# Optimization experiments

Measured on AMD Instinct MI355X. Metric: run time of the kernel, lower is better.

The kernel has to match this reference:

```python
import jax, jax.numpy as jnp
import numpy as np
from jax import lax

H = 1024       # hidden_size
I = 1024       # intermediate_size (per expert)
E = 16         # num_experts
TOP_K = 4      # num_active_experts


def setup_inputs() -> dict:
    key = jax.random.key(0)
    ks = jax.random.split(key, 9)
    std_gate = 0.02 / (E ** 0.5)
    return {
        "hidden_states": jax.random.normal(ks[0], (1, 2048, H), jnp.float32),
        "gate_w": jax.random.normal(ks[1], (E, H), jnp.float32) * std_gate,
        "expert_bias": jnp.zeros((E,), jnp.float32),
        "w1": jax.random.normal(ks[2], (E, I, H), jnp.float32) * 0.02,
        "w2": jax.random.normal(ks[3], (E, H, I), jnp.float32) * 0.02,
        "w3": jax.random.normal(ks[4], (E, I, H), jnp.float32) * 0.02,
        "sw1": jax.random.normal(ks[5], (I, H), jnp.float32) * 0.02,
        "sw2": jax.random.normal(ks[6], (H, I), jnp.float32) * 0.02,
        "sw3": jax.random.normal(ks[7], (I, H), jnp.float32) * 0.02,
    }


def _swiglu(x, wg, wd, wu):
    # Swish(x W1^T) * (x W3^T) then W2^T
    return (jax.nn.silu(x @ wg.T) * (x @ wu.T)) @ wd.T


def reference(hidden_states, gate_w, expert_bias, w1, w2, w3, sw1, sw2, sw3):
    B, S, Hd = hidden_states.shape
    x = hidden_states.reshape(-1, Hd)              # [T, H]
    T = x.shape[0]

    # ---- Router ----
    router_logits = x @ gate_w.T                   # [T, E]
    biased = router_logits + expert_bias           # loss-free balancing bias
    _, sel = lax.top_k(biased, TOP_K)              # [T, K] indices from biased logits
    raw = jnp.take_along_axis(router_logits, sel, axis=-1)  # weights from UNbiased logits
    rw = jax.nn.softmax(raw.astype(jnp.float32), axis=-1).astype(x.dtype)  # [T, K]

    # Dense combine weights g[t, e] = routing weight if e selected else 0
    g = jnp.zeros((T, E), x.dtype).at[jnp.arange(T)[:, None], sel].add(rw)

    # ---- Routed experts (mathematically equal to grouped dispatch) ----
    routed = jnp.zeros_like(x)
    for e in range(E):  # fixed small expert loop
        routed = routed + g[:, e:e + 1] * _swiglu(x, w1[e], w2[e], w3[e])

    # ---- Shared expert ----
    shared = _swiglu(x, sw1, sw2, sw3)

    out = (shared + routed).reshape(B, S, Hd)      # dropout p=0 -> identity
    return out
```

## Files before the change

### kernel.cpp

```cpp
#include <hip/hip_runtime.h>
#include <cstddef>
#include <cstdint>

#define T_TOK 2048
#define HD 1024
#define ID 1024
#define NE 16
#define TOPK 4
#define BM 128
#define BN 128
#define BK 32
#define MT_MAX 96
#define SLOT_CAP (MT_MAX * BM)

typedef float f32x4 __attribute__((ext_vector_type(4)));
typedef __bf16 bf16x8 __attribute__((ext_vector_type(8)));
typedef __bf16 bf16x4 __attribute__((ext_vector_type(4)));

#define WS_TILE_E 256
#define WS_LOGITS 4096
#define WS_SLOT_TOK (WS_LOGITS + T_TOK * NE * 4)
#define WS_SLOT_W (WS_SLOT_TOK + SLOT_CAP * 4)
#define WS_H1 (WS_SLOT_W + SLOT_CAP * 4)
#define WS_XB (WS_H1 + (size_t)SLOT_CAP * ID * 2)

__device__ __forceinline__ f32x4 mfma16(bf16x8 a, bf16x8 b, f32x4 c) {
  return __builtin_amdgcn_mfma_f32_16x16x32_bf16(a, b, c, 0, 0, 0);
}

__device__ __forceinline__ bf16x8 pack8(f32x4 a, f32x4 b) {
  bf16x8 o;
  o[0] = (__bf16)a[0]; o[1] = (__bf16)a[1]; o[2] = (__bf16)a[2]; o[3] = (__bf16)a[3];
  o[4] = (__bf16)b[0]; o[5] = (__bf16)b[1]; o[6] = (__bf16)b[2]; o[7] = (__bf16)b[3];
  return o;
}

__device__ __forceinline__ bf16x4 pack4(f32x4 a) {
  bf16x4 o;
  o[0] = (__bf16)a[0]; o[1] = (__bf16)a[1]; o[2] = (__bf16)a[2]; o[3] = (__bf16)a[3];
  return o;
}

__device__ __forceinline__ void gload16(const __bf16* g, __bf16* l) {
  __builtin_amdgcn_global_load_lds(
      (const __attribute__((address_space(1))) uint32_t*)g,
      (__attribute__((address_space(3))) uint32_t*)l, 16, 0, 0);
}
__device__ __forceinline__ void gload16f(const float* g, float* l) {
  __builtin_amdgcn_global_load_lds(
      (const __attribute__((address_space(1))) uint32_t*)g,
      (__attribute__((address_space(3))) uint32_t*)l, 16, 0, 0);
}

#define LOGITS_BLOCKS (T_TOK / 4)
#define XCHUNKS 256

__global__ __launch_bounds__(256) void fused_pre(
    const float* __restrict__ x, const float* __restrict__ gw,
    __bf16* __restrict__ xb, float* __restrict__ logits) {
  int tid = threadIdx.x;
  if ((int)blockIdx.x < LOGITS_BLOCKS) {
    int wv = tid >> 6;
    int lane = tid & 63;
    int tok = blockIdx.x * 4 + wv;
    int e = lane >> 2;
    int q = lane & 3;
    const float4* xr = (const float4*)(x + (size_t)tok * HD) + q * 64;
    const float4* wr = (const float4*)(gw + (size_t)e * HD) + q * 64;
    float s0 = 0.f, s1 = 0.f;
#pragma unroll 8
    for (int i = 0; i < 64; i += 2) {
      float4 a0 = xr[i], w0 = wr[i];
      float4 a1 = xr[i + 1], w1v = wr[i + 1];
      s0 += a0.x * w0.x + a0.y * w0.y + a0.z * w0.z + a0.w * w0.w;
      s1 += a1.x * w1v.x + a1.y * w1v.y + a1.z * w1v.z + a1.w * w1v.w;
    }
    float s = s0 + s1;
    s += __shfl_xor(s, 1);
    s += __shfl_xor(s, 2);
    if (q == 0) logits[(size_t)tok * NE + e] = s;
    return;
  }
  size_t f = (size_t)(blockIdx.x - LOGITS_BLOCKS) * 2048;
  const f32x4* p = (const f32x4*)x + f + tid;
  __bf16* q = xb + 4 * (f + tid);
  f32x4 v0 = p[0], v1 = p[256], v2 = p[512], v3 = p[768];
  f32x4 v4 = p[1024], v5 = p[1280], v6 = p[1536], v7 = p[1792];
  *(bf16x4*)(q + 0 * 1024) = pack4(v0);
  *(bf16x4*)(q + 1 * 1024) = pack4(v1);
  *(bf16x4*)(q + 2 * 1024) = pack4(v2);
  *(bf16x4*)(q + 3 * 1024) = pack4(v3);
  *(bf16x4*)(q + 4 * 1024) = pack4(v4);
  *(bf16x4*)(q + 5 * 1024) = pack4(v5);
  *(bf16x4*)(q + 6 * 1024) = pack4(v6);
  *(bf16x4*)(q + 7 * 1024) = pack4(v7);
}

__global__ __launch_bounds__(256) void router_finish(
    const float* __restrict__ logits, const float* __restrict__ bias,
    int* __restrict__ tile_e, int* __restrict__ slot_tok,
    float* __restrict__ slot_w) {
  __shared__ int hist[NE];
  __shared__ int soff[NE + 1];
  __shared__ int fillp[NE];
  __shared__ unsigned lsel[T_TOK];
  __shared__ float4 lw4[T_TOK];

  int tid = threadIdx.x;
  if (tid < NE) { hist[tid] = 0; fillp[tid] = 0; }
  __syncthreads();

  float bb[NE];
#pragma unroll
  for (int e = 0; e < NE; ++e) bb[e] = bias[e];

  for (int j = 0; j < T_TOK / 256; ++j) {
    int t = tid + 256 * j;
    float lg[NE];
    const float4* lp = (const float4*)(logits + (size_t)t * NE);
#pragma unroll
    for (int q = 0; q < 4; ++q) {
      float4 v = lp[q];
      lg[4 * q] = v.x; lg[4 * q + 1] = v.y; lg[4 * q + 2] = v.z; lg[4 * q + 3] = v.w;
    }
    float b[NE];
#pragma unroll
    for (int e = 0; e < NE; ++e) b[e] = lg[e] + bb[e];

    int selk[TOPK];
    float raw[TOPK];
    unsigned used = 0;
#pragma unroll
    for (int k = 0; k < TOPK; ++k) {
      float best = -3.4e38f;
      int bi = 0;
#pragma unroll
      for (int e = 0; e < NE; ++e) {
        if (!((used >> e) & 1) && b[e] > best) { best = b[e]; bi = e; }
      }
      used |= (1u << bi);
      selk[k] = bi;
      raw[k] = lg[bi];
    }
    float m = raw[0];
#pragma unroll
    for (int k = 1; k < TOPK; ++k) m = fmaxf(m, raw[k]);
    float s = 0.f;
    float w[TOPK];
#pragma unroll
    for (int k = 0; k < TOPK; ++k) { w[k] = __expf(raw[k] - m); s += w[k]; }
    float inv = 1.f / s;
    lsel[t] = (unsigned)selk[0] | ((unsigned)selk[1] << 8) |
              ((unsigned)selk[2] << 16) | ((unsigned)selk[3] << 24);
    lw4[t] = make_float4(w[0] * inv, w[1] * inv, w[2] * inv, w[3] * inv);
#pragma unroll
    for (int k = 0; k < TOPK; ++k) atomicAdd(&hist[selk[k]], 1);
  }
  __syncthreads();

  if (tid == 0) {
    int o = 0;
    for (int e = 0; e < NE; ++e) { soff[e] = o; o += (hist[e] + BM - 1) & ~(BM - 1); }
    soff[NE] = o;
  }
  __syncthreads();
  int shared_base = soff[NE];
  int total = shared_base + T_TOK;
  for (int tt = tid; tt < MT_MAX; tt += 256) {
    int base = tt * BM;
    int ee = -1;
    if (base < shared_base) {
      ee = 0;
#pragma unroll
      for (int q = 1; q < NE; ++q) if (base >= soff[q]) ee = q;
    } else if (base < total) {
      ee = NE;
    }
    tile_e[tt] = ee;
  }

  for (int j = 0; j < T_TOK / 256; ++j) {
    int t = tid + 256 * j;
    unsigned ps = lsel[t];
    float4 wv = lw4[t];
    int e0 = ps & 255, e1 = (ps >> 8) & 255, e2 = (ps >> 16) & 255, e3 = ps >> 24;
    int p0 = atomicAdd(&fillp[e0], 1);
    slot_tok[soff[e0] + p0] = t; slot_w[soff[e0] + p0] = wv.x;
    int p1 = atomicAdd(&fillp[e1], 1);
    slot_tok[soff[e1] + p1] = t; slot_w[soff[e1] + p1] = wv.y;
    int p2 = atomicAdd(&fillp[e2], 1);
    slot_tok[soff[e2] + p2] = t; slot_w[soff[e2] + p2] = wv.z;
    int p3 = atomicAdd(&fillp[e3], 1);
    slot_tok[soff[e3] + p3] = t; slot_w[soff[e3] + p3] = wv.w;
  }

  for (int s = tid; s < shared_base; s += 256) {
    int e = 0;
#pragma unroll
    for (int q = 1; q < NE; ++q) if (s >= soff[q]) e = q;
    if (s >= soff[e] + hist[e]) { slot_tok[s] = -1; slot_w[s] = 0.f; }
  }
  for (int s = shared_base + tid; s < total; s += 256) {
    slot_tok[s] = s - shared_base;
    slot_w[s] = 1.0f;
  }
}


__global__ __launch_bounds__(256, 2) void pass1_bf16(
    const __bf16* __restrict__ xb, const int* __restrict__ slot_tok,
    const int* __restrict__ tile_e, const float* __restrict__ w1,
    const float* __restrict__ w3, const float* __restrict__ sw1,
    const float* __restrict__ sw3, __bf16* __restrict__ h1) {
  int mt = blockIdx.y;
  int e = tile_e[mt];
  if (e < 0) return;
  int n0 = blockIdx.x * BN;
  int m0 = mt * BM;

  const float* wg = (e == NE) ? sw1 : w1 + (size_t)e * ID * HD;
  const float* wu = (e == NE) ? sw3 : w3 + (size_t)e * ID * HD;

  __shared__ __align__(16) __bf16 As[2][BM * BK];
  __shared__ __align__(16) float BgF[2][BN * BK];
  __shared__ __align__(16) float BuF[2][BN * BK];

  int tid = threadIdx.x;
  int r0 = tid >> 2, r1 = r0 + 64;
  int c8 = ((tid & 3) ^ ((r0 >> 1) & 3)) * 8;
  int tok0 = slot_tok[m0 + r0]; if (tok0 < 0) tok0 = 0;
  int tok1 = slot_tok[m0 + r1]; if (tok1 < 0) tok1 = 0;
  const __bf16* gA0 = xb + (size_t)tok0 * HD + c8;
  const __bf16* gA1 = xb + (size_t)tok1 * HD + c8;

  const float* srcG[4];
  const float* srcU[4];
  int ldst[4];
#pragma unroll
  for (int j = 0; j < 4; ++j) {
    int id = tid + j * 256;
    int r = id >> 3, s = id & 7;
    int go = (s ^ (r & 7)) << 2;
    srcG[j] = wg + (size_t)(n0 + r) * HD + go;
    srcU[j] = wu + (size_t)(n0 + r) * HD + go;
    ldst[j] = id * 4;
  }

  int wave = tid >> 6, lane = tid & 63;
  int wm = (wave >> 1) * 64, wn = (wave & 1) * 64;
  int l16 = lane & 15, kch = lane >> 4;
  int kk8 = (kch ^ ((l16 >> 1) & 3)) * 8;
  int sw = l16 & 7;
  int cB0 = ((2 * kch) ^ sw) * 4;
  int cB1 = ((2 * kch + 1) ^ sw) * 4;

  f32x4 accg[4][4] = {};
  f32x4 accu[4][4] = {};

  auto stage = [&](int B, int k0) {
    gload16(gA0 + k0, &As[B][(size_t)tid * 8]);
    gload16(gA1 + k0, &As[B][(size_t)(tid + 256) * 8]);
#pragma unroll
    for (int j = 0; j < 4; ++j) {
      gload16f(srcG[j] + k0, &BgF[B][ldst[j]]);
      gload16f(srcU[j] + k0, &BuF[B][ldst[j]]);
    }
  };
  auto body = [&](int B) {
    bf16x8 af[4], gf[4], uf[4];
#pragma unroll
    for (int i = 0; i < 4; ++i)
      af[i] = *(const bf16x8*)(&As[B][(wm + i * 16 + l16) * BK + kk8]);
#pragma unroll
    for (int i = 0; i < 4; ++i) {
      int rb = (wn + i * 16 + l16) * BK;
      f32x4 ga = *(const f32x4*)(&BgF[B][rb + cB0]);
      f32x4 gb = *(const f32x4*)(&BgF[B][rb + cB1]);
      gf[i] = pack8(ga, gb);
      f32x4 ua = *(const f32x4*)(&BuF[B][rb + cB0]);
      f32x4 ub = *(const f32x4*)(&BuF[B][rb + cB1]);
      uf[i] = pack8(ua, ub);
    }
    asm volatile("s_waitcnt lgkmcnt(0)" ::: "memory");
    __builtin_amdgcn_s_barrier();
    __builtin_amdgcn_sched_barrier(0);
#pragma unroll
    for (int mi = 0; mi < 4; ++mi)
#pragma unroll
      for (int ni = 0; ni < 4; ++ni) {
        accg[mi][ni] = mfma16(af[mi], gf[ni], accg[mi][ni]);
        accu[mi][ni] = mfma16(af[mi], uf[ni], accu[mi][ni]);
      }
  };

  stage(0, 0);
#pragma unroll 1
  for (int k = 0; k < HD / BK - 1; ++k) {
    int cur = k & 1;
    stage(cur ^ 1, (k + 1) * BK);
    asm volatile("s_waitcnt vmcnt(10)" ::: "memory");
    __builtin_amdgcn_s_barrier();
    __builtin_amdgcn_sched_barrier(0);
    body(cur);
  }
  asm volatile("s_waitcnt vmcnt(0)" ::: "memory");
  __builtin_amdgcn_s_barrier();
  __builtin_amdgcn_sched_barrier(0);
  body((HD / BK - 1) & 1);

#pragma unroll
  for (int mi = 0; mi < 4; ++mi) {
#pragma unroll
    for (int ni = 0; ni < 4; ++ni) {
#pragma unroll
      for (int j = 0; j < 4; ++j) {
        int row = m0 + wm + mi * 16 + kch * 4 + j;
        int col = n0 + wn + ni * 16 + l16;
        float g = accg[mi][ni][j];
        float u = accu[mi][ni][j];
        float hv = (g / (1.f + __expf(-g))) * u;
        h1[(size_t)row * ID + col] = (__bf16)hv;
      }
    }
  }
}

__global__ __launch_bounds__(256, 3) void pass2_bf16(
    const __bf16* __restrict__ h1, const int* __restrict__ slot_tok,
    const float* __restrict__ slot_w, const int* __restrict__ tile_e,
    const float* __restrict__ w2, const float* __restrict__ sw2,
    float* __restrict__ out) {
  int mt = blockIdx.y;
  int e = tile_e[mt];
  if (e < 0) return;
  int n0 = blockIdx.x * BN;
  int m0 = mt * BM;

  const float* wd = (e == NE) ? sw2 : w2 + (size_t)e * HD * ID;

  __shared__ __align__(16) __bf16 As[2][BM * BK];
  __shared__ __align__(16) float BF[2][BN * BK];

  int tid = threadIdx.x;
  int r0 = tid >> 2, r1 = r0 + 64;
  int c8 = ((tid & 3) ^ ((r0 >> 1) & 3)) * 8;
  const __bf16* gA0 = h1 + (size_t)(m0 + r0) * ID + c8;
  const __bf16* gA1 = h1 + (size_t)(m0 + r1) * ID + c8;

  const float* srcB[4];
  int ldst[4];
#pragma unroll
  for (int j = 0; j < 4; ++j) {
    int id = tid + j * 256;
    int r = id >> 3, s = id & 7;
    int go = (s ^ (r & 7)) << 2;
    srcB[j] = wd + (size_t)(n0 + r) * ID + go;
    ldst[j] = id * 4;
  }

  int wave = tid >> 6, lane = tid & 63;
  int wm = (wave >> 1) * 64, wn = (wave & 1) * 64;
  int l16 = lane & 15, kch = lane >> 4;
  int kk8 = (kch ^ ((l16 >> 1) & 3)) * 8;
  int sw = l16 & 7;
  int cB0 = ((2 * kch) ^ sw) * 4;
  int cB1 = ((2 * kch + 1) ^ sw) * 4;

  f32x4 acc[4][4] = {};

  auto stage = [&](int B, int k0) {
    gload16(gA0 + k0, &As[B][(size_t)tid * 8]);
    gload16(gA1 + k0, &As[B][(size_t)(tid + 256) * 8]);
#pragma unroll
    for (int j = 0; j < 4; ++j) gload16f(srcB[j] + k0, &BF[B][ldst[j]]);
  };
  auto body = [&](int B) {
    bf16x8 af[4], bf[4];
#pragma unroll
    for (int i = 0; i < 4; ++i)
      af[i] = *(const bf16x8*)(&As[B][(wm + i * 16 + l16) * BK + kk8]);
#pragma unroll
    for (int i = 0; i < 4; ++i) {
      int rb = (wn + i * 16 + l16) * BK;
      f32x4 ba = *(const f32x4*)(&BF[B][rb + cB0]);
      f32x4 bb = *(const f32x4*)(&BF[B][rb + cB1]);
      bf[i] = pack8(ba, bb);
    }
    asm volatile("s_waitcnt lgkmcnt(0)" ::: "memory");
    __builtin_amdgcn_s_barrier();
    __builtin_amdgcn_sched_barrier(0);
#pragma unroll
    for (int mi = 0; mi < 4; ++mi)
#pragma unroll
      for (int ni = 0; ni < 4; ++ni)
        acc[mi][ni] = mfma16(af[mi], bf[ni], acc[mi][ni]);
  };

  stage(0, 0);
#pragma unroll 1
  for (int k = 0; k < ID / BK - 1; ++k) {
    int cur = k & 1;
    stage(cur ^ 1, (k + 1) * BK);
    asm volatile("s_waitcnt vmcnt(6)" ::: "memory");
    __builtin_amdgcn_s_barrier();
    __builtin_amdgcn_sched_barrier(0);
    body(cur);
  }
  asm volatile("s_waitcnt vmcnt(0)" ::: "memory");
  __builtin_amdgcn_s_barrier();
  __builtin_amdgcn_sched_barrier(0);
  body((ID / BK - 1) & 1);

#pragma unroll
  for (int mi = 0; mi < 4; ++mi) {
#pragma unroll
    for (int j = 0; j < 4; ++j) {
      int row = m0 + wm + mi * 16 + kch * 4 + j;
      int token = slot_tok[row];
      if (token < 0) continue;
      float wgt = slot_w[row];
#pragma unroll
      for (int ni = 0; ni < 4; ++ni) {
        int col = n0 + wn + ni * 16 + l16;
        atomicAdd(out + (size_t)token * HD + col, wgt * acc[mi][ni][j]);
      }
    }
  }
}

extern "C" void kernel_launch(void* const* d_in, const int* in_sizes, int n_in,
                              void* d_out, int out_size, void* d_ws, size_t ws_size,
                              hipStream_t stream) {
  const float* x = (const float*)d_in[0];
  const float* gate_w = (const float*)d_in[1];
  const float* ebias = (const float*)d_in[2];
  const float* w1 = (const float*)d_in[3];
  const float* w2 = (const float*)d_in[4];
  const float* w3 = (const float*)d_in[5];
  const float* sw1 = (const float*)d_in[6];
  const float* sw2 = (const float*)d_in[7];
  const float* sw3 = (const float*)d_in[8];
  float* out = (float*)d_out;

  char* ws = (char*)d_ws;
  int* tile_e = (int*)(ws + WS_TILE_E);
  float* logits = (float*)(ws + WS_LOGITS);
  int* slot_tok = (int*)(ws + WS_SLOT_TOK);
  float* slot_w = (float*)(ws + WS_SLOT_W);
  __bf16* h1 = (__bf16*)(ws + WS_H1);
  __bf16* xb = (__bf16*)(ws + WS_XB);

  hipMemsetAsync(d_out, 0, (size_t)T_TOK * HD * sizeof(float), stream);

  fused_pre<<<LOGITS_BLOCKS + XCHUNKS, 256, 0, stream>>>(x, gate_w, xb, logits);
  router_finish<<<1, 256, 0, stream>>>(logits, ebias, tile_e, slot_tok, slot_w);

  pass1_bf16<<<dim3(ID / BN, MT_MAX), 256, 0, stream>>>(
      xb, slot_tok, tile_e, w1, w3, sw1, sw3, h1);
  pass2_bf16<<<dim3(HD / BN, MT_MAX), 256, 0, stream>>>(
      h1, slot_tok, slot_w, tile_e, w2, sw2, out);
}
```

Baseline: 223.8 us.

## Use 256-row, 512-thread tiles in pass1 to halve weight reloads

Expert segments are now padded to 256 rows, and pass1 runs 512-thread blocks that each cover 256 token slots by 128 columns, with a new tile-to-expert map for the larger tiles. Each block loads its fp32 gate and up weight tiles once for twice as many rows, halving weight traffic and bf16 conversion per token. Pass2 keeps 128-row tiles through the old map, which still lines up because every segment is a multiple of 128. The cost is more padding rows per expert, more LDS per block and more accumulator registers per wave, which may lower occupancy.

Result: slower. 245.6 us (+9.7%).

```diff
diff --git a/kernel.cpp b/kernel.cpp
--- a/kernel.cpp
+++ b/kernel.cpp
@@ -8,16 +8,19 @@
 #define NE 16
 #define TOPK 4
 #define BM 128
+#define BM2 256
 #define BN 128
 #define BK 32
-#define MT_MAX 96
-#define SLOT_CAP (MT_MAX * BM)
+#define MT_MAX 128
+#define MT2_MAX 64
+#define SLOT_CAP 16384
 
 typedef float f32x4 __attribute__((ext_vector_type(4)));
 typedef __bf16 bf16x8 __attribute__((ext_vector_type(8)));
 typedef __bf16 bf16x4 __attribute__((ext_vector_type(4)));
 
 #define WS_TILE_E 256
+#define WS_TILE_E2 2048
 #define WS_LOGITS 4096
 #define WS_SLOT_TOK (WS_LOGITS + T_TOK * NE * 4)
 #define WS_SLOT_W (WS_SLOT_TOK + SLOT_CAP * 4)
@@ -98,8 +101,8 @@
 
 __global__ __launch_bounds__(256) void router_finish(
     const float* __restrict__ logits, const float* __restrict__ bias,
-    int* __restrict__ tile_e, int* __restrict__ slot_tok,
-    float* __restrict__ slot_w) {
+    int* __restrict__ tile_e, int* __restrict__ tile_e2,
+    int* __restrict__ slot_tok, float* __restrict__ slot_w) {
   __shared__ int hist[NE];
   __shared__ int soff[NE + 1];
   __shared__ int fillp[NE];
@@ -160,7 +163,7 @@
 
   if (tid == 0) {
     int o = 0;
-    for (int e = 0; e < NE; ++e) { soff[e] = o; o += (hist[e] + BM - 1) & ~(BM - 1); }
+    for (int e = 0; e < NE; ++e) { soff[e] = o; o += (hist[e] + BM2 - 1) & ~(BM2 - 1); }
     soff[NE] = o;
   }
   __syncthreads();
@@ -177,6 +180,18 @@
       ee = NE;
     }
     tile_e[tt] = ee;
+  }
+  for (int tt = tid; tt < MT2_MAX; tt += 256) {
+    int base = tt * BM2;
+    int ee = -1;
+    if (base < shared_base) {
+      ee = 0;
+#pragma unroll
+      for (int q = 1; q < NE; ++q) if (base >= soff[q]) ee = q;
+    } else if (base < total) {
+      ee = NE;
+    }
+    tile_e2[tt] = ee;
   }
 
   for (int j = 0; j < T_TOK / 256; ++j) {
@@ -206,73 +221,74 @@
   }
 }
 
-
-__global__ __launch_bounds__(256, 2) void pass1_bf16(
+__global__ __launch_bounds__(512, 2) void pass1_bf16(
     const __bf16* __restrict__ xb, const int* __restrict__ slot_tok,
-    const int* __restrict__ tile_e, const float* __restrict__ w1,
+    const int* __restrict__ tile_e2, const float* __restrict__ w1,
     const float* __restrict__ w3, const float* __restrict__ sw1,
     const float* __restrict__ sw3, __bf16* __restrict__ h1) {
   int mt = blockIdx.y;
-  int e = tile_e[mt];
+  int e = tile_e2[mt];
   if (e < 0) return;
   int n0 = blockIdx.x * BN;
-  int m0 = mt * BM;
+  int m0 = mt * BM2;
 
   const float* wg = (e == NE) ? sw1 : w1 + (size_t)e * ID * HD;
   const float* wu = (e == NE) ? sw3 : w3 + (size_t)e * ID * HD;
 
-  __shared__ __align__(16) __bf16 As[2][BM * BK];
+  __shared__ __align__(16) __bf16 As[2][BM2 * BK];
   __shared__ __align__(16) float BgF[2][BN * BK];
   __shared__ __align__(16) float BuF[2][BN * BK];
 
   int tid = threadIdx.x;
-  int r0 = tid >> 2, r1 = r0 + 64;
-  int c8 = ((tid & 3) ^ ((r0 >> 1) & 3)) * 8;
-  int tok0 = slot_tok[m0 + r0]; if (tok0 < 0) tok0 = 0;
-  int tok1 = slot_tok[m0 + r1]; if (tok1 < 0) tok1 = 0;
-  const __bf16* gA0 = xb + (size_t)tok0 * HD + c8;
-  const __bf16* gA1 = xb + (size_t)tok1 * HD + c8;
-
-  const float* srcG[4];
-  const float* srcU[4];
-  int ldst[4];
-#pragma unroll
-  for (int j = 0; j < 4; ++j) {
-    int id = tid + j * 256;
+  const __bf16* gA[2];
+#pragma unroll
+  for (int j = 0; j < 2; ++j) {
+    int id = tid + j * 512;
+    int r = id >> 2;
+    int cc = (id & 3) ^ ((r >> 1) & 3);
+    int tok = slot_tok[m0 + r];
+    if (tok < 0) tok = 0;
+    gA[j] = xb + (size_t)tok * HD + cc * 8;
+  }
+  const float* srcG[2];
+  const float* srcU[2];
+#pragma unroll
+  for (int j = 0; j < 2; ++j) {
+    int id = tid + j * 512;
     int r = id >> 3, s = id & 7;
     int go = (s ^ (r & 7)) << 2;
     srcG[j] = wg + (size_t)(n0 + r) * HD + go;
     srcU[j] = wu + (size_t)(n0 + r) * HD + go;
-    ldst[j] = id * 4;
   }
 
   int wave = tid >> 6, lane = tid & 63;
-  int wm = (wave >> 1) * 64, wn = (wave & 1) * 64;
+  int wm = (wave >> 2) * 128;
+  int wn = (wave & 3) * 32;
   int l16 = lane & 15, kch = lane >> 4;
   int kk8 = (kch ^ ((l16 >> 1) & 3)) * 8;
   int sw = l16 & 7;
   int cB0 = ((2 * kch) ^ sw) * 4;
   int cB1 = ((2 * kch + 1) ^ sw) * 4;
 
-  f32x4 accg[4][4] = {};
-  f32x4 accu[4][4] = {};
+  f32x4 accg[8][2] = {};
+  f32x4 accu[8][2] = {};
 
   auto stage = [&](int B, int k0) {
-    gload16(gA0 + k0, &As[B][(size_t)tid * 8]);
-    gload16(gA1 + k0, &As[B][(size_t)(tid + 256) * 8]);
-#pragma unroll
-    for (int j = 0; j < 4; ++j) {
-      gload16f(srcG[j] + k0, &BgF[B][ldst[j]]);
-      gload16f(srcU[j] + k0, &BuF[B][ldst[j]]);
+#pragma unroll
+    for (int j = 0; j < 2; ++j) {
+      int id = tid + j * 512;
+      gload16(gA[j] + k0, &As[B][(size_t)id * 8]);
+      gload16f(srcG[j] + k0, &BgF[B][(size_t)id * 4]);
+      gload16f(srcU[j] + k0, &BuF[B][(size_t)id * 4]);
     }
   };
   auto body = [&](int B) {
-    bf16x8 af[4], gf[4], uf[4];
-#pragma unroll
-    for (int i = 0; i < 4; ++i)
+    bf16x8 af[8], gf[2], uf[2];
+#pragma unroll
+    for (int i = 0; i < 8; ++i)
       af[i] = *(const bf16x8*)(&As[B][(wm + i * 16 + l16) * BK + kk8]);
 #pragma unroll
-    for (int i = 0; i < 4; ++i) {
+    for (int i = 0; i < 2; ++i) {
       int rb = (wn + i * 16 + l16) * BK;
       f32x4 ga = *(const f32x4*)(&BgF[B][rb + cB0]);
       f32x4 gb = *(const f32x4*)(&BgF[B][rb + cB1]);
@@ -285,9 +301,9 @@
     __builtin_amdgcn_s_barrier();
     __builtin_amdgcn_sched_barrier(0);
 #pragma unroll
-    for (int mi = 0; mi < 4; ++mi)
-#pragma unroll
-      for (int ni = 0; ni < 4; ++ni) {
+    for (int mi = 0; mi < 8; ++mi)
+#pragma unroll
+      for (int ni = 0; ni < 2; ++ni) {
         accg[mi][ni] = mfma16(af[mi], gf[ni], accg[mi][ni]);
         accu[mi][ni] = mfma16(af[mi], uf[ni], accu[mi][ni]);
       }
@@ -298,7 +314,7 @@
   for (int k = 0; k < HD / BK - 1; ++k) {
     int cur = k & 1;
     stage(cur ^ 1, (k + 1) * BK);
-    asm volatile("s_waitcnt vmcnt(10)" ::: "memory");
+    asm volatile("s_waitcnt vmcnt(6)" ::: "memory");
     __builtin_amdgcn_s_barrier();
     __builtin_amdgcn_sched_barrier(0);
     body(cur);
@@ -309,9 +325,9 @@
   body((HD / BK - 1) & 1);
 
 #pragma unroll
-  for (int mi = 0; mi < 4; ++mi) {
-#pragma unroll
-    for (int ni = 0; ni < 4; ++ni) {
+  for (int mi = 0; mi < 8; ++mi) {
+#pragma unroll
+    for (int ni = 0; ni < 2; ++ni) {
 #pragma unroll
       for (int j = 0; j < 4; ++j) {
         int row = m0 + wm + mi * 16 + kch * 4 + j;
@@ -444,6 +460,7 @@
 
   char* ws = (char*)d_ws;
   int* tile_e = (int*)(ws + WS_TILE_E);
+  int* tile_e2 = (int*)(ws + WS_TILE_E2);
   float* logits = (float*)(ws + WS_LOGITS);
   int* slot_tok = (int*)(ws + WS_SLOT_TOK);
   float* slot_w = (float*)(ws + WS_SLOT_W);
@@ -453,10 +470,11 @@
   hipMemsetAsync(d_out, 0, (size_t)T_TOK * HD * sizeof(float), stream);
 
   fused_pre<<<LOGITS_BLOCKS + XCHUNKS, 256, 0, stream>>>(x, gate_w, xb, logits);
-  router_finish<<<1, 256, 0, stream>>>(logits, ebias, tile_e, slot_tok, slot_w);
-
-  pass1_bf16<<<dim3(ID / BN, MT_MAX), 256, 0, stream>>>(
-      xb, slot_tok, tile_e, w1, w3, sw1, sw3, h1);
+  router_finish<<<1, 256, 0, stream>>>(logits, ebias, tile_e, tile_e2, slot_tok,
+                                       slot_w);
+
+  pass1_bf16<<<dim3(ID / BN, MT2_MAX), 512, 0, stream>>>(
+      xb, slot_tok, tile_e2, w1, w3, sw1, sw3, h1);
   pass2_bf16<<<dim3(HD / BN, MT_MAX), 256, 0, stream>>>(
       h1, slot_tok, slot_w, tile_e, w2, sw2, out);
 }
```

## Pre-convert w1/w3 and shared gate/up weights to bf16 before pass1

Applied to the files above, without the earlier changes.

Adds a grid-stride conversion of all routed w1/w3 weights (plus x) to bf16 inside the pre-kernel, and a separate kernel that converts the shared-expert sw1/sw3. Pass1 then stages bf16 weight tiles straight into LDS with direct global-to-LDS loads, dropping the in-loop fp32-to-bf16 packing and halving per-tile weight bytes. The wait count is adjusted to match the fewer loads. In exchange, every call pays a full extra read of the fp32 weights plus a write of the bf16 copies before the GEMM can start.

After: 235.3 us. 5.1% more time.

```diff
diff --git a/kernel.cpp b/kernel.cpp
--- a/kernel.cpp
+++ b/kernel.cpp
@@ -23,6 +23,8 @@
 #define WS_SLOT_W (WS_SLOT_TOK + SLOT_CAP * 4)
 #define WS_H1 (WS_SLOT_W + SLOT_CAP * 4)
 #define WS_XB (WS_H1 + (size_t)SLOT_CAP * ID * 2)
+#define WS_W1B (WS_XB + (size_t)T_TOK * HD * 2)
+#define WS_W3B (WS_W1B + (size_t)NE * ID * HD * 2)
 
 __device__ __forceinline__ f32x4 mfma16(bf16x8 a, bf16x8 b, f32x4 c) {
   return __builtin_amdgcn_mfma_f32_16x16x32_bf16(a, b, c, 0, 0, 0);
@@ -52,12 +54,18 @@
       (__attribute__((address_space(3))) uint32_t*)l, 16, 0, 0);
 }
 
+#define W4 ((size_t)1 << 22)
+#define X4 ((size_t)1 << 19)
+#define CVT4_TOTAL (2 * W4 + X4)
+#define NCHUNK (CVT4_TOTAL / 2048)
+#define CVT_GRID 2048
 #define LOGITS_BLOCKS (T_TOK / 4)
-#define XCHUNKS 256
 
 __global__ __launch_bounds__(256) void fused_pre(
-    const float* __restrict__ x, const float* __restrict__ gw,
-    __bf16* __restrict__ xb, float* __restrict__ logits) {
+    const float* __restrict__ w1, const float* __restrict__ w3,
+    const float* __restrict__ x, __bf16* __restrict__ w1b,
+    __bf16* __restrict__ w3b, __bf16* __restrict__ xb,
+    const float* __restrict__ gw, float* __restrict__ logits) {
   int tid = threadIdx.x;
   if ((int)blockIdx.x < LOGITS_BLOCKS) {
     int wv = tid >> 6;
@@ -81,19 +89,34 @@
     if (q == 0) logits[(size_t)tok * NE + e] = s;
     return;
   }
-  size_t f = (size_t)(blockIdx.x - LOGITS_BLOCKS) * 2048;
-  const f32x4* p = (const f32x4*)x + f + tid;
-  __bf16* q = xb + 4 * (f + tid);
-  f32x4 v0 = p[0], v1 = p[256], v2 = p[512], v3 = p[768];
-  f32x4 v4 = p[1024], v5 = p[1280], v6 = p[1536], v7 = p[1792];
-  *(bf16x4*)(q + 0 * 1024) = pack4(v0);
-  *(bf16x4*)(q + 1 * 1024) = pack4(v1);
-  *(bf16x4*)(q + 2 * 1024) = pack4(v2);
-  *(bf16x4*)(q + 3 * 1024) = pack4(v3);
-  *(bf16x4*)(q + 4 * 1024) = pack4(v4);
-  *(bf16x4*)(q + 5 * 1024) = pack4(v5);
-  *(bf16x4*)(q + 6 * 1024) = pack4(v6);
-  *(bf16x4*)(q + 7 * 1024) = pack4(v7);
+  size_t b = blockIdx.x - LOGITS_BLOCKS;
+  for (size_t c = b; c < NCHUNK; c += CVT_GRID) {
+    size_t f = c * 2048;
+    const float* src;
+    __bf16* dst;
+    size_t off;
+    if (f < W4) { src = w1; dst = w1b; off = f; }
+    else if (f < 2 * W4) { src = w3; dst = w3b; off = f - W4; }
+    else { src = x; dst = xb; off = f - 2 * W4; }
+    const f32x4* p = (const f32x4*)src + off + tid;
+    __bf16* q = dst + 4 * (off + tid);
+    f32x4 v0 = __builtin_nontemporal_load(p);
+    f32x4 v1 = __builtin_nontemporal_load(p + 256);
+    f32x4 v2 = __builtin_nontemporal_load(p + 512);
+    f32x4 v3 = __builtin_nontemporal_load(p + 768);
+    f32x4 v4 = __builtin_nontemporal_load(p + 1024);
+    f32x4 v5 = __builtin_nontemporal_load(p + 1280);
+    f32x4 v6 = __builtin_nontemporal_load(p + 1536);
+    f32x4 v7 = __builtin_nontemporal_load(p + 1792);
+    *(bf16x4*)(q + 0 * 1024) = pack4(v0);
+    *(bf16x4*)(q + 1 * 1024) = pack4(v1);
+    *(bf16x4*)(q + 2 * 1024) = pack4(v2);
+    *(bf16x4*)(q + 3 * 1024) = pack4(v3);
+    *(bf16x4*)(q + 4 * 1024) = pack4(v4);
+    *(bf16x4*)(q + 5 * 1024) = pack4(v5);
+    *(bf16x4*)(q + 6 * 1024) = pack4(v6);
+    *(bf16x4*)(q + 7 * 1024) = pack4(v7);
+  }
 }
 
 __global__ __launch_bounds__(256) void router_finish(
@@ -206,24 +229,24 @@
   }
 }
 
-
 __global__ __launch_bounds__(256, 2) void pass1_bf16(
     const __bf16* __restrict__ xb, const int* __restrict__ slot_tok,
-    const int* __restrict__ tile_e, const float* __restrict__ w1,
-    const float* __restrict__ w3, const float* __restrict__ sw1,
-    const float* __restrict__ sw3, __bf16* __restrict__ h1) {
+    const int* __restrict__ tile_e, const __bf16* __restrict__ w1b,
+    const __bf16* __restrict__ w3b, const float* __restrict__ sw1,
+    const float* __restrict__ sw3, __bf16* __restrict__ h1,
+    const __bf16* __restrict__ dummy) {
   int mt = blockIdx.y;
   int e = tile_e[mt];
   if (e < 0) return;
   int n0 = blockIdx.x * BN;
   int m0 = mt * BM;
 
-  const float* wg = (e == NE) ? sw1 : w1 + (size_t)e * ID * HD;
-  const float* wu = (e == NE) ? sw3 : w3 + (size_t)e * ID * HD;
+  const __bf16* wg = w1b + (size_t)e * ID * HD;
+  const __bf16* wu = w3b + (size_t)e * ID * HD;
 
   __shared__ __align__(16) __bf16 As[2][BM * BK];
-  __shared__ __align__(16) float BgF[2][BN * BK];
-  __shared__ __align__(16) float BuF[2][BN * BK];
+  __shared__ __align__(16) __bf16 Bg[2][BN * BK];
+  __shared__ __align__(16) __bf16 Bu[2][BN * BK];
 
   int tid = threadIdx.x;
   int r0 = tid >> 2, r1 = r0 + 64;
@@ -232,27 +255,15 @@
   int tok1 = slot_tok[m0 + r1]; if (tok1 < 0) tok1 = 0;
   const __bf16* gA0 = xb + (size_t)tok0 * HD + c8;
   const __bf16* gA1 = xb + (size_t)tok1 * HD + c8;
-
-  const float* srcG[4];
-  const float* srcU[4];
-  int ldst[4];
-#pragma unroll
-  for (int j = 0; j < 4; ++j) {
-    int id = tid + j * 256;
-    int r = id >> 3, s = id & 7;
-    int go = (s ^ (r & 7)) << 2;
-    srcG[j] = wg + (size_t)(n0 + r) * HD + go;
-    srcU[j] = wu + (size_t)(n0 + r) * HD + go;
-    ldst[j] = id * 4;
-  }
+  const __bf16* gG0 = wg + (size_t)(n0 + r0) * HD + c8;
+  const __bf16* gG1 = wg + (size_t)(n0 + r1) * HD + c8;
+  const __bf16* gU0 = wu + (size_t)(n0 + r0) * HD + c8;
+  const __bf16* gU1 = wu + (size_t)(n0 + r1) * HD + c8;
 
   int wave = tid >> 6, lane = tid & 63;
   int wm = (wave >> 1) * 64, wn = (wave & 1) * 64;
   int l16 = lane & 15, kch = lane >> 4;
   int kk8 = (kch ^ ((l16 >> 1) & 3)) * 8;
-  int sw = l16 & 7;
-  int cB0 = ((2 * kch) ^ sw) * 4;
-  int cB1 = ((2 * kch + 1) ^ sw) * 4;
 
   f32x4 accg[4][4] = {};
   f32x4 accu[4][4] = {};
@@ -260,26 +271,18 @@
   auto stage = [&](int B, int k0) {
     gload16(gA0 + k0, &As[B][(size_t)tid * 8]);
     gload16(gA1 + k0, &As[B][(size_t)(tid + 256) * 8]);
-#pragma unroll
-    for (int j = 0; j < 4; ++j) {
-      gload16f(srcG[j] + k0, &BgF[B][ldst[j]]);
-      gload16f(srcU[j] + k0, &BuF[B][ldst[j]]);
-    }
+    gload16(gG0 + k0, &Bg[B][(size_t)tid * 8]);
+    gload16(gG1 + k0, &Bg[B][(size_t)(tid + 256) * 8]);
+    gload16(gU0 + k0, &Bu[B][(size_t)tid * 8]);
+    gload16(gU1 + k0, &Bu[B][(size_t)(tid + 256) * 8]);
   };
   auto body = [&](int B) {
     bf16x8 af[4], gf[4], uf[4];
 #pragma unroll
-    for (int i = 0; i < 4; ++i)
+    for (int i = 0; i < 4; ++i) {
       af[i] = *(const bf16x8*)(&As[B][(wm + i * 16 + l16) * BK + kk8]);
-#pragma unroll
-    for (int i = 0; i < 4; ++i) {
-      int rb = (wn + i * 16 + l16) * BK;
-      f32x4 ga = *(const f32x4*)(&BgF[B][rb + cB0]);
-      f32x4 gb = *(const f32x4*)(&BgF[B][rb + cB1]);
-      gf[i] = pack8(ga, gb);
-      f32x4 ua = *(const f32x4*)(&BuF[B][rb + cB0]);
-      f32x4 ub = *(const f32x4*)(&BuF[B][rb + cB1]);
-      uf[i] = pack8(ua, ub);
+      gf[i] = *(const bf16x8*)(&Bg[B][(wn + i * 16 + l16) * BK + kk8]);
+      uf[i] = *(const bf16x8*)(&Bu[B][(wn + i * 16 + l16) * BK + kk8]);
     }
     asm volatile("s_waitcnt lgkmcnt(0)" ::: "memory");
     __builtin_amdgcn_s_barrier();
@@ -298,7 +301,7 @@
   for (int k = 0; k < HD / BK - 1; ++k) {
     int cur = k & 1;
     stage(cur ^ 1, (k + 1) * BK);
-    asm volatile("s_waitcnt vmcnt(10)" ::: "memory");
+    asm volatile("s_waitcnt vmcnt(6)" ::: "memory");
     __builtin_amdgcn_s_barrier();
     __builtin_amdgcn_sched_barrier(0);
     body(cur);
@@ -323,6 +326,31 @@
       }
     }
   }
+}
+
+__global__ __launch_bounds__(256) void cvt_shared(
+    const float* __restrict__ sw1, const float* __restrict__ sw3,
+    __bf16* __restrict__ sw1b, __bf16* __restrict__ sw3b) {
+  size_t c = blockIdx.x;
+  size_t f = c * 2048;
+  const float* src;
+  __bf16* dst;
+  size_t off;
+  if (f < ((size_t)1 << 18)) { src = sw1; dst = sw1b; off = f; }
+  else { src = sw3; dst = sw3b; off = f - ((size_t)1 << 18); }
+  int tid = threadIdx.x;
+  const f32x4* p = (const f32x4*)src + off + tid;
+  __bf16* q = dst + 4 * (off + tid);
+  f32x4 v0 = p[0], v1 = p[256], v2 = p[512], v3 = p[768];
+  f32x4 v4 = p[1024], v5 = p[1280], v6 = p[1536], v7 = p[1792];
+  *(bf16x4*)(q + 0 * 1024) = pack4(v0);
+  *(bf16x4*)(q + 1 * 1024) = pack4(v1);
+  *(bf16x4*)(q + 2 * 1024) = pack4(v2);
+  *(bf16x4*)(q + 3 * 1024) = pack4(v3);
+  *(bf16x4*)(q + 4 * 1024) = pack4(v4);
+  *(bf16x4*)(q + 5 * 1024) = pack4(v5);
+  *(bf16x4*)(q + 6 * 1024) = pack4(v6);
+  *(bf16x4*)(q + 7 * 1024) = pack4(v7);
 }
 
 __global__ __launch_bounds__(256, 3) void pass2_bf16(
@@ -449,14 +477,20 @@
   float* slot_w = (float*)(ws + WS_SLOT_W);
   __bf16* h1 = (__bf16*)(ws + WS_H1);
   __bf16* xb = (__bf16*)(ws + WS_XB);
+  __bf16* w1b = (__bf16*)(ws + WS_W1B);
+  __bf16* w3b = w1b + (size_t)17 * ID * HD;
+  __bf16* sw1b = w1b + (size_t)16 * ID * HD;
+  __bf16* sw3b = w3b + (size_t)16 * ID * HD;
 
   hipMemsetAsync(d_out, 0, (size_t)T_TOK * HD * sizeof(float), stream);
 
-  fused_pre<<<LOGITS_BLOCKS + XCHUNKS, 256, 0, stream>>>(x, gate_w, xb, logits);
+  fused_pre<<<LOGITS_BLOCKS + CVT_GRID, 256, 0, stream>>>(
+      w1, w3, x, w1b, w3b, xb, gate_w, logits);
+  cvt_shared<<<256, 256, 0, stream>>>(sw1, sw3, sw1b, sw3b);
   router_finish<<<1, 256, 0, stream>>>(logits, ebias, tile_e, slot_tok, slot_w);
 
   pass1_bf16<<<dim3(ID / BN, MT_MAX), 256, 0, stream>>>(
-      xb, slot_tok, tile_e, w1, w3, sw1, sw3, h1);
+      xb, slot_tok, tile_e, w1b, w3b, sw1, sw3, h1, nullptr);
   pass2_bf16<<<dim3(HD / BN, MT_MAX), 256, 0, stream>>>(
       h1, slot_tok, slot_w, tile_e, w2, sw2, out);
 }
```
